# Optimization experiments

Measured on AMD Instinct MI355X. Metric: run time of the kernel, lower is better.

## Reference

```python
import jax, jax.numpy as jnp
import numpy as np

ALPHA = 0.01
BETA = 3e-05
OUT_H, OUT_W = 256, 256
KSIZE, SIGMA = 5, 4.0


def _gaussian_kernel2d(ks=KSIZE, sigma=SIGMA):
    x = jnp.arange(ks, dtype=jnp.float32) - (ks - 1) / 2.0
    g = jnp.exp(-(x * x) / (2.0 * sigma * sigma))
    g = g / g.sum()
    return jnp.outer(g, g)  # [ks, ks]


def _gaussian_blur(maps):
    # maps: [B, H, W]; reflect padding + depthwise 5x5 gaussian (kornia-style GaussianBlur2d)
    k = _gaussian_kernel2d()[None, None]  # [1,1,5,5]
    p = KSIZE // 2
    x = jnp.pad(maps[:, None], ((0, 0), (0, 0), (p, p), (p, p)), mode='reflect')
    y = jax.lax.conv_general_dilated(x, k, (1, 1), 'VALID')
    return y[:, 0]


def _resize_bilinear_align_corners(x, oh, ow):
    # x: [B, h, w] -> [B, oh, ow], torch F.interpolate(mode='bilinear', align_corners=True)
    B, h, w = x.shape
    ys = jnp.linspace(0.0, h - 1.0, oh)
    xs = jnp.linspace(0.0, w - 1.0, ow)
    y0 = jnp.floor(ys).astype(jnp.int32)
    x0 = jnp.floor(xs).astype(jnp.int32)
    y1 = jnp.minimum(y0 + 1, h - 1)
    x1 = jnp.minimum(x0 + 1, w - 1)
    fy = (ys - y0.astype(ys.dtype))[:, None]  # [oh,1]
    fx = (xs - x0.astype(xs.dtype))[None, :]  # [1,ow]
    a = x[:, y0][:, :, x0]
    b = x[:, y0][:, :, x1]
    c = x[:, y1][:, :, x0]
    d = x[:, y1][:, :, x1]
    top = a * (1.0 - fx) + b * fx
    bot = c * (1.0 - fx) + d * fx
    return top * (1.0 - fy) + bot * fy


def setup_inputs() -> dict:
    key = jax.random.key(0)
    k0, k1, k2 = jax.random.split(key, 3)
    B = 256
    return {
        'out0': jax.random.normal(k0, (B, 64, 64), jnp.float32),
        'out1': jax.random.normal(k1, (B, 32, 32), jnp.float32),
        'out2': jax.random.normal(k2, (B, 16, 16), jnp.float32),
    }


def reference(out0, out1, out2):
    outputs = [out0, out1, out2]
    B = out0.shape[0]
    # per-sample max of each scale -> softmax-weighted selection of per-sample weight
    max_vals = jnp.stack([o.reshape(B, -1).max(axis=1) for o in outputs], axis=1)  # [B,3]
    probs = jax.nn.softmax(max_vals, axis=1)
    mask = probs > probs.mean(axis=1, keepdims=True)  # probs > prob_mean
    cnt = mask.sum(axis=1)
    sel_mean = (max_vals * mask).sum(axis=1) / jnp.maximum(cnt, 1)
    total_weights = jnp.where(cnt > 0, jnp.maximum(sel_mean * ALPHA, BETA), BETA)  # [B]
    # multi-scale fusion: bilinear(align_corners=True) upsample to (256,256) and sum
    maps = _resize_bilinear_align_corners(out0, OUT_H, OUT_W)
    maps = maps + _resize_bilinear_align_corners(out1, OUT_H, OUT_W)
    maps = maps + _resize_bilinear_align_corners(out2, OUT_H, OUT_W)
    # gaussian blur then per-sample score. torch takes topk(k=f(total_weights)).values[0],
    # and topk values are sorted descending, so values[0] == max (k / total_weights drop out).
    blurred = _gaussian_blur(maps)
    scores = blurred.reshape(B, -1).max(axis=1)
    del total_weights  # only influenced the (unused) top-k size in the original
    return scores[:, None], maps
```

## Files before the change

### kernel.cpp

```cpp
#include <hip/hip_runtime.h>
#include <math.h>


static constexpr int W  = 256;
static constexpr int QH = 4;

__device__ __forceinline__ int reflect256(int i) {
    if (i < 0) i = -i;
    if (i > 255) i = 510 - i;
    return i;
}

__global__ __launch_bounds__(256, 4) void fused_kernel(
    const float* __restrict__ in0,
    const float* __restrict__ in1,
    const float* __restrict__ in2,
    float* __restrict__ part,
    float* __restrict__ maps)
{
    const int t   = threadIdx.x;
    const int q   = t & 63;
    const int wv  = __builtin_amdgcn_readfirstlane(t >> 6);
    const int bid = blockIdx.x;
    const int b   = bid >> 2;
    const int r0  = (bid & 3) * 64;
    const int rw0 = r0 + wv * 16;
    const int c0  = q * 4;

    __shared__ float s0[64 * 64];
    __shared__ float s1[32 * 32];
    __shared__ float s2[16 * 16];
    __shared__ float red[4];

    {
        const float4* g0 = (const float4*)(in0 + (size_t)b * 4096);
        const float4* g1 = (const float4*)(in1 + (size_t)b * 1024);
        const float4* g2 = (const float4*)(in2 + (size_t)b * 256);
        float4* l0 = (float4*)s0;
        float4* l1 = (float4*)s1;
        float4* l2 = (float4*)s2;
#pragma unroll
        for (int i = 0; i < 4; ++i) l0[t + i * 256] = g0[t + i * 256];
        l1[t] = g1[t];
        if (t < 64) l2[t] = g2[t];
    }
    __syncthreads();

    const float inv255 = 1.0f / 255.0f;
    int x00[4]; float fx0[4];
    int x10[4]; float fx1[4];
    int x20[4]; float fx2[4];
#pragma unroll
    for (int k = 0; k < 4; ++k) {
        const int c = c0 + k;
        int ix = c * 63; x00[k] = ix / 255; fx0[k] = (float)(ix - 255 * x00[k]) * inv255;
        ix = c * 31;     x10[k] = ix / 255; fx1[k] = (float)(ix - 255 * x10[k]) * inv255;
        ix = c * 15;     x20[k] = ix / 255; fx2[k] = (float)(ix - 255 * x20[k]) * inv255;
    }

    auto xq0 = [&](int y, float* o) {
        const float* row = s0 + y * 64;
#pragma unroll
        for (int k = 0; k < 4; ++k) {
            int xa = x00[k], xb = min(xa + 1, 63);
            float a = row[xa], bb = row[xb];
            o[k] = a + fx0[k] * (bb - a);
        }
    };
    auto xq1 = [&](int y, float* o) {
        const float* row = s1 + y * 32;
#pragma unroll
        for (int k = 0; k < 4; ++k) {
            int xa = x10[k], xb = min(xa + 1, 31);
            float a = row[xa], bb = row[xb];
            o[k] = a + fx1[k] * (bb - a);
        }
    };
    auto xq2 = [&](int y, float* o) {
        const float* row = s2 + y * 16;
#pragma unroll
        for (int k = 0; k < 4; ++k) {
            int xa = x20[k], xb = min(xa + 1, 15);
            float a = row[xa], bb = row[xb];
            o[k] = a + fx2[k] * (bb - a);
        }
    };

    auto direct4 = [&](int rn, float* o) {
        const int ry = reflect256(rn);
        int iy0 = ry * 63; int ya0 = iy0 / 255; float fya = (float)(iy0 - 255 * ya0) * inv255; int ya1 = min(ya0 + 1, 63);
        int iy1 = ry * 31; int yb0 = iy1 / 255; float fyb = (float)(iy1 - 255 * yb0) * inv255; int yb1 = min(yb0 + 1, 31);
        int iy2 = ry * 15; int yc0 = iy2 / 255; float fyc = (float)(iy2 - 255 * yc0) * inv255; int yc1 = min(yc0 + 1, 15);
        const float* r0a = s0 + ya0 * 64; const float* r0b = s0 + ya1 * 64;
        const float* r1a = s1 + yb0 * 32; const float* r1b = s1 + yb1 * 32;
        const float* r2a = s2 + yc0 * 16; const float* r2b = s2 + yc1 * 16;
#pragma unroll
        for (int k = 0; k < 4; ++k) {
            int xa = x00[k], xb = min(xa + 1, 63);
            float a = r0a[xa], bv = r0a[xb], cv = r0b[xa], dv = r0b[xb];
            float top = a + fx0[k] * (bv - a);
            float bot = cv + fx0[k] * (dv - cv);
            float v = top + fya * (bot - top);
            xa = x10[k]; xb = min(xa + 1, 31);
            a = r1a[xa]; bv = r1a[xb]; cv = r1b[xa]; dv = r1b[xb];
            top = a + fx1[k] * (bv - a);
            bot = cv + fx1[k] * (dv - cv);
            v += top + fyb * (bot - top);
            xa = x20[k]; xb = min(xa + 1, 15);
            a = r2a[xa]; bv = r2a[xb]; cv = r2b[xa]; dv = r2b[xb];
            top = a + fx2[k] * (bv - a);
            bot = cv + fx2[k] * (dv - cv);
            v += top + fyc * (bot - top);
            o[k] = v;
        }
    };

    const float e1 = expf(-1.0f / 32.0f);
    const float e2 = expf(-4.0f / 32.0f);
    const float nrm = 1.0f + 2.0f * e1 + 2.0f * e2;
    const float gwc = 1.0f / nrm, gwa = e1 / nrm, gwb = e2 / nrm;

    float m0[4], m1[4], m2[4], m3[4], mn[4];
    direct4(rw0 - 2, m0);
    direct4(rw0 - 1, m1);
    direct4(rw0,     m2);
    direct4(rw0 + 1, m3);

    float* __restrict__ mpr = maps + ((size_t)b * W + (size_t)rw0) * W + c0;
    *(float4*)(mpr)     = make_float4(m2[0], m2[1], m2[2], m2[3]);
    *(float4*)(mpr + W) = make_float4(m3[0], m3[1], m3[2], m3[3]);

    int iy, ya, yb, yc, rem0, rem1, rem2;
    float rlo0[4], rhi0[4], rlo1[4], rhi1[4], rlo2[4], rhi2[4];
    iy = (rw0 + 2) * 63; ya = iy / 255; rem0 = iy - 255 * ya; xq0(ya, rlo0); xq0(min(ya + 1, 63), rhi0);
    iy = (rw0 + 2) * 31; yb = iy / 255; rem1 = iy - 255 * yb; xq1(yb, rlo1); xq1(min(yb + 1, 31), rhi1);
    iy = (rw0 + 2) * 15; yc = iy / 255; rem2 = iy - 255 * yc; xq2(yc, rlo2); xq2(min(yc + 1, 15), rhi2);

    float gmax = -INFINITY;

#pragma unroll 4
    for (int i = 0; i < 16; ++i) {
        const int rn = rw0 + 2 + i;
        if (rn <= 255) {
            const float w0 = (float)rem0 * inv255;
            const float w1 = (float)rem1 * inv255;
            const float w2 = (float)rem2 * inv255;
#pragma unroll
            for (int k = 0; k < 4; ++k) {
                float v0 = rlo0[k] + w0 * (rhi0[k] - rlo0[k]);
                float v1 = rlo1[k] + w1 * (rhi1[k] - rlo1[k]);
                float v2 = rlo2[k] + w2 * (rhi2[k] - rlo2[k]);
                mn[k] = v0 + v1 + v2;
            }
            rem0 += 63;
            if (rem0 >= 255) {
                rem0 -= 255; ++ya;
#pragma unroll
                for (int k = 0; k < 4; ++k) rlo0[k] = rhi0[k];
                xq0(min(ya + 1, 63), rhi0);
            }
            rem1 += 31;
            if (rem1 >= 255) {
                rem1 -= 255; ++yb;
#pragma unroll
                for (int k = 0; k < 4; ++k) rlo1[k] = rhi1[k];
                xq1(min(yb + 1, 31), rhi1);
            }
            rem2 += 15;
            if (rem2 >= 255) {
                rem2 -= 255; ++yc;
#pragma unroll
                for (int k = 0; k < 4; ++k) rlo2[k] = rhi2[k];
                xq2(min(yc + 1, 15), rhi2);
            }
        } else {
            direct4(rn, mn);
        }

        if (i < 14)
            *(float4*)(mpr + (size_t)(2 + i) * W) = make_float4(mn[0], mn[1], mn[2], mn[3]);

        float vr0 = gwb * (m0[0] + mn[0]) + gwa * (m1[0] + m3[0]) + gwc * m2[0];
        float vr1 = gwb * (m0[1] + mn[1]) + gwa * (m1[1] + m3[1]) + gwc * m2[1];
        float vr2 = gwb * (m0[2] + mn[2]) + gwa * (m1[2] + m3[2]) + gwc * m2[2];
        float vr3 = gwb * (m0[3] + mn[3]) + gwa * (m1[3] + m3[3]) + gwc * m2[3];
#pragma unroll
        for (int k = 0; k < 4; ++k) { m0[k] = m1[k]; m1[k] = m2[k]; m2[k] = m3[k]; m3[k] = mn[k]; }

        float az = __shfl_up(vr2, 1);
        float aw = __shfl_up(vr3, 1);
        float cx = __shfl_down(vr0, 1);
        float cy = __shfl_down(vr1, 1);
        float a2 = (q == 0)  ? vr2 : az;
        float a3 = (q == 0)  ? vr1 : aw;
        float c4 = (q == 63) ? vr2 : cx;
        float c5 = (q == 63) ? vr1 : cy;
        float o0 = gwc * vr0 + gwa * (a3 + vr1)  + gwb * (a2 + vr2);
        float o1 = gwc * vr1 + gwa * (vr0 + vr2) + gwb * (a3 + vr3);
        float o2 = gwc * vr2 + gwa * (vr1 + vr3) + gwb * (vr0 + c4);
        float o3 = gwc * vr3 + gwa * (vr2 + c4)  + gwb * (vr1 + c5);
        gmax = fmaxf(gmax, fmaxf(fmaxf(o0, o1), fmaxf(o2, o3)));
    }

#pragma unroll
    for (int off = 32; off > 0; off >>= 1)
        gmax = fmaxf(gmax, __shfl_down(gmax, off));
    if (q == 0) red[wv] = gmax;
    __syncthreads();
    if (t == 0)
        part[bid] = fmaxf(fmaxf(red[0], red[1]), fmaxf(red[2], red[3]));
}

__global__ void reduce_kernel(const float* __restrict__ part,
                              float* __restrict__ scores, int B) {
    int i = blockIdx.x * blockDim.x + threadIdx.x;
    if (i < B) {
        float m = part[QH * i];
#pragma unroll
        for (int k = 1; k < QH; ++k) m = fmaxf(m, part[QH * i + k]);
        scores[i] = m;
    }
}

extern "C" void kernel_launch(void* const* d_in, const int* in_sizes, int n_in,
                              void* d_out, int out_size, void* d_ws, size_t ws_size,
                              hipStream_t stream) {
    const float* in0 = (const float*)d_in[0];
    const float* in1 = (const float*)d_in[1];
    const float* in2 = (const float*)d_in[2];
    const int B = in_sizes[0] / (64 * 64);

    float* scores = (float*)d_out;
    float* maps   = (float*)d_out + B;
    float* part   = (float*)d_ws;

    hipLaunchKernelGGL(fused_kernel, dim3(B * QH), dim3(256), 0, stream,
                       in0, in1, in2, part, maps);
    hipLaunchKernelGGL(reduce_kernel, dim3((B + 255) / 256), dim3(256), 0, stream,
                       part, scores, B);
}
```

Measured before the change: 109.4 us.

## Split each sample into eight row bands and stage only needed input rows

Each block now covers 32 output rows instead of 64, with 8 rows per wave, doubling the grid and raising launch bounds to 8 blocks per CU. Only the source rows each band touches are copied into a much smaller LDS buffer, which cuts LDS use and redundant global loads. The halo rows are now produced by the incremental stepping interpolator instead of direct 4-tap evaluation, with a reflect special case for row 0. Per-wave maxima are written straight to the workspace, removing the block barrier, and the reduce kernel now reads 32 partials per sample.

After: 267.4 us. 145% more time.

```diff
diff --git a/kernel.cpp b/kernel.cpp
--- a/kernel.cpp
+++ b/kernel.cpp
@@ -3,7 +3,7 @@
 
 
 static constexpr int W  = 256;
-static constexpr int QH = 4;
+static constexpr int QB = 8;
 
 __device__ __forceinline__ int reflect256(int i) {
     if (i < 0) i = -i;
@@ -11,7 +11,7 @@
     return i;
 }
 
-__global__ __launch_bounds__(256, 4) void fused_kernel(
+__global__ __launch_bounds__(256, 8) void fused_kernel(
     const float* __restrict__ in0,
     const float* __restrict__ in1,
     const float* __restrict__ in2,
@@ -22,27 +22,34 @@
     const int q   = t & 63;
     const int wv  = __builtin_amdgcn_readfirstlane(t >> 6);
     const int bid = blockIdx.x;
-    const int b   = bid >> 2;
-    const int r0  = (bid & 3) * 64;
-    const int rw0 = r0 + wv * 16;
+    const int b   = bid >> 3;
+    const int r0  = (bid & 7) * 32;
+    const int rw0 = r0 + wv * 8;
     const int c0  = q * 4;
 
-    __shared__ float s0[64 * 64];
-    __shared__ float s1[32 * 32];
-    __shared__ float s2[16 * 16];
-    __shared__ float red[4];
+    const int rlo = max(r0 - 2, 0);
+    const int rhi = min(r0 + 33, 255);
+    const int y0lo = (rlo * 63) / 255;
+    const int y1lo = (rlo * 31) / 255;
+    const int y2lo = (rlo * 15) / 255;
+    const int y0hi = min((rhi * 63) / 255 + 1, 63);
+    const int y1hi = min((rhi * 31) / 255 + 1, 31);
+    const int y2hi = min((rhi * 15) / 255 + 1, 15);
+
+    __shared__ float s0[11 * 64];
+    __shared__ float s1[7 * 32];
+    __shared__ float s2[5 * 16];
 
     {
-        const float4* g0 = (const float4*)(in0 + (size_t)b * 4096);
-        const float4* g1 = (const float4*)(in1 + (size_t)b * 1024);
-        const float4* g2 = (const float4*)(in2 + (size_t)b * 256);
-        float4* l0 = (float4*)s0;
-        float4* l1 = (float4*)s1;
-        float4* l2 = (float4*)s2;
-#pragma unroll
-        for (int i = 0; i < 4; ++i) l0[t + i * 256] = g0[t + i * 256];
-        l1[t] = g1[t];
-        if (t < 64) l2[t] = g2[t];
+        const float4* g0 = (const float4*)(in0 + (size_t)b * 4096 + y0lo * 64);
+        const float4* g1 = (const float4*)(in1 + (size_t)b * 1024 + y1lo * 32);
+        const float4* g2 = (const float4*)(in2 + (size_t)b * 256  + y2lo * 16);
+        const int n0 = (y0hi - y0lo + 1) * 16;
+        const int n1 = (y1hi - y1lo + 1) * 8;
+        const int n2 = (y2hi - y2lo + 1) * 4;
+        if (t < n0) ((float4*)s0)[t] = g0[t];
+        if (t < n1) ((float4*)s1)[t] = g1[t];
+        if (t < n2) ((float4*)s2)[t] = g2[t];
     }
     __syncthreads();
 
@@ -59,7 +66,7 @@
     }
 
     auto xq0 = [&](int y, float* o) {
-        const float* row = s0 + y * 64;
+        const float* row = s0 + (y - y0lo) * 64;
 #pragma unroll
         for (int k = 0; k < 4; ++k) {
             int xa = x00[k], xb = min(xa + 1, 63);
@@ -68,7 +75,7 @@
         }
     };
     auto xq1 = [&](int y, float* o) {
-        const float* row = s1 + y * 32;
+        const float* row = s1 + (y - y1lo) * 32;
 #pragma unroll
         for (int k = 0; k < 4; ++k) {
             int xa = x10[k], xb = min(xa + 1, 31);
@@ -77,7 +84,7 @@
         }
     };
     auto xq2 = [&](int y, float* o) {
-        const float* row = s2 + y * 16;
+        const float* row = s2 + (y - y2lo) * 16;
 #pragma unroll
         for (int k = 0; k < 4; ++k) {
             int xa = x20[k], xb = min(xa + 1, 15);
@@ -91,9 +98,9 @@
         int iy0 = ry * 63; int ya0 = iy0 / 255; float fya = (float)(iy0 - 255 * ya0) * inv255; int ya1 = min(ya0 + 1, 63);
         int iy1 = ry * 31; int yb0 = iy1 / 255; float fyb = (float)(iy1 - 255 * yb0) * inv255; int yb1 = min(yb0 + 1, 31);
         int iy2 = ry * 15; int yc0 = iy2 / 255; float fyc = (float)(iy2 - 255 * yc0) * inv255; int yc1 = min(yc0 + 1, 15);
-        const float* r0a = s0 + ya0 * 64; const float* r0b = s0 + ya1 * 64;
-        const float* r1a = s1 + yb0 * 32; const float* r1b = s1 + yb1 * 32;
-        const float* r2a = s2 + yc0 * 16; const float* r2b = s2 + yc1 * 16;
+        const float* r0a = s0 + (ya0 - y0lo) * 64; const float* r0b = s0 + (ya1 - y0lo) * 64;
+        const float* r1a = s1 + (yb0 - y1lo) * 32; const float* r1b = s1 + (yb1 - y1lo) * 32;
+        const float* r2a = s2 + (yc0 - y2lo) * 16; const float* r2b = s2 + (yc1 - y2lo) * 16;
 #pragma unroll
         for (int k = 0; k < 4; ++k) {
             int xa = x00[k], xb = min(xa + 1, 63);
@@ -115,69 +122,81 @@
         }
     };
 
+    int ya, yb, yc, rem0, rem1, rem2;
+    float rl0[4], rh0[4], rl1[4], rh1[4], rl2[4], rh2[4];
+
+    auto init_state = [&](int rn) {
+        int iy;
+        iy = rn * 63; ya = iy / 255; rem0 = iy - 255 * ya; xq0(ya, rl0); xq0(min(ya + 1, 63), rh0);
+        iy = rn * 31; yb = iy / 255; rem1 = iy - 255 * yb; xq1(yb, rl1); xq1(min(yb + 1, 31), rh1);
+        iy = rn * 15; yc = iy / 255; rem2 = iy - 255 * yc; xq2(yc, rl2); xq2(min(yc + 1, 15), rh2);
+    };
+
+    auto step = [&](float* o) {
+        const float w0 = (float)rem0 * inv255;
+        const float w1 = (float)rem1 * inv255;
+        const float w2 = (float)rem2 * inv255;
+#pragma unroll
+        for (int k = 0; k < 4; ++k) {
+            float v0 = rl0[k] + w0 * (rh0[k] - rl0[k]);
+            float v1 = rl1[k] + w1 * (rh1[k] - rl1[k]);
+            float v2 = rl2[k] + w2 * (rh2[k] - rl2[k]);
+            o[k] = v0 + v1 + v2;
+        }
+        rem0 += 63;
+        if (rem0 >= 255) {
+            rem0 -= 255; ++ya;
+#pragma unroll
+            for (int k = 0; k < 4; ++k) rl0[k] = rh0[k];
+            xq0(min(ya + 1, 63), rh0);
+        }
+        rem1 += 31;
+        if (rem1 >= 255) {
+            rem1 -= 255; ++yb;
+#pragma unroll
+            for (int k = 0; k < 4; ++k) rl1[k] = rh1[k];
+            xq1(min(yb + 1, 31), rh1);
+        }
+        rem2 += 15;
+        if (rem2 >= 255) {
+            rem2 -= 255; ++yc;
+#pragma unroll
+            for (int k = 0; k < 4; ++k) rl2[k] = rh2[k];
+            xq2(min(yc + 1, 15), rh2);
+        }
+    };
+
     const float e1 = expf(-1.0f / 32.0f);
     const float e2 = expf(-4.0f / 32.0f);
     const float nrm = 1.0f + 2.0f * e1 + 2.0f * e2;
     const float gwc = 1.0f / nrm, gwa = e1 / nrm, gwb = e2 / nrm;
 
     float m0[4], m1[4], m2[4], m3[4], mn[4];
-    direct4(rw0 - 2, m0);
-    direct4(rw0 - 1, m1);
-    direct4(rw0,     m2);
-    direct4(rw0 + 1, m3);
+    if (rw0 == 0) {
+        direct4(2, m0);
+        direct4(1, m1);
+        direct4(0, m2);
+#pragma unroll
+        for (int k = 0; k < 4; ++k) m3[k] = m1[k];
+        init_state(2);
+    } else {
+        init_state(rw0 - 2);
+        step(m0); step(m1); step(m2); step(m3);
+    }
 
     float* __restrict__ mpr = maps + ((size_t)b * W + (size_t)rw0) * W + c0;
     *(float4*)(mpr)     = make_float4(m2[0], m2[1], m2[2], m2[3]);
     *(float4*)(mpr + W) = make_float4(m3[0], m3[1], m3[2], m3[3]);
 
-    int iy, ya, yb, yc, rem0, rem1, rem2;
-    float rlo0[4], rhi0[4], rlo1[4], rhi1[4], rlo2[4], rhi2[4];
-    iy = (rw0 + 2) * 63; ya = iy / 255; rem0 = iy - 255 * ya; xq0(ya, rlo0); xq0(min(ya + 1, 63), rhi0);
-    iy = (rw0 + 2) * 31; yb = iy / 255; rem1 = iy - 255 * yb; xq1(yb, rlo1); xq1(min(yb + 1, 31), rhi1);
-    iy = (rw0 + 2) * 15; yc = iy / 255; rem2 = iy - 255 * yc; xq2(yc, rlo2); xq2(min(yc + 1, 15), rhi2);
-
     float gmax = -INFINITY;
 
-#pragma unroll 4
-    for (int i = 0; i < 16; ++i) {
+#pragma unroll
+    for (int i = 0; i < 8; ++i) {
         const int rn = rw0 + 2 + i;
-        if (rn <= 255) {
-            const float w0 = (float)rem0 * inv255;
-            const float w1 = (float)rem1 * inv255;
-            const float w2 = (float)rem2 * inv255;
-#pragma unroll
-            for (int k = 0; k < 4; ++k) {
-                float v0 = rlo0[k] + w0 * (rhi0[k] - rlo0[k]);
-                float v1 = rlo1[k] + w1 * (rhi1[k] - rlo1[k]);
-                float v2 = rlo2[k] + w2 * (rhi2[k] - rlo2[k]);
-                mn[k] = v0 + v1 + v2;
-            }
-            rem0 += 63;
-            if (rem0 >= 255) {
-                rem0 -= 255; ++ya;
-#pragma unroll
-                for (int k = 0; k < 4; ++k) rlo0[k] = rhi0[k];
-                xq0(min(ya + 1, 63), rhi0);
-            }
-            rem1 += 31;
-            if (rem1 >= 255) {
-                rem1 -= 255; ++yb;
-#pragma unroll
-                for (int k = 0; k < 4; ++k) rlo1[k] = rhi1[k];
-                xq1(min(yb + 1, 31), rhi1);
-            }
-            rem2 += 15;
-            if (rem2 >= 255) {
-                rem2 -= 255; ++yc;
-#pragma unroll
-                for (int k = 0; k < 4; ++k) rlo2[k] = rhi2[k];
-                xq2(min(yc + 1, 15), rhi2);
-            }
-        } else {
-            direct4(rn, mn);
-        }
-
-        if (i < 14)
+        if (rn <= 255) step(mn);
+        else           direct4(rn, mn);
+
+        if (i < 6)
             *(float4*)(mpr + (size_t)(2 + i) * W) = make_float4(mn[0], mn[1], mn[2], mn[3]);
 
         float vr0 = gwb * (m0[0] + mn[0]) + gwa * (m1[0] + m3[0]) + gwc * m2[0];
@@ -205,19 +224,20 @@
 #pragma unroll
     for (int off = 32; off > 0; off >>= 1)
         gmax = fmaxf(gmax, __shfl_down(gmax, off));
-    if (q == 0) red[wv] = gmax;
-    __syncthreads();
-    if (t == 0)
-        part[bid] = fmaxf(fmaxf(red[0], red[1]), fmaxf(red[2], red[3]));
+    if (q == 0) part[bid * 4 + wv] = gmax;
 }
 
 __global__ void reduce_kernel(const float* __restrict__ part,
                               float* __restrict__ scores, int B) {
     int i = blockIdx.x * blockDim.x + threadIdx.x;
     if (i < B) {
-        float m = part[QH * i];
-#pragma unroll
-        for (int k = 1; k < QH; ++k) m = fmaxf(m, part[QH * i + k]);
+        const float4* p = (const float4*)(part + 32 * i);
+        float m = -INFINITY;
+#pragma unroll
+        for (int k = 0; k < 8; ++k) {
+            float4 v = p[k];
+            m = fmaxf(m, fmaxf(fmaxf(v.x, v.y), fmaxf(v.z, v.w)));
+        }
         scores[i] = m;
     }
 }
@@ -234,7 +254,7 @@
     float* maps   = (float*)d_out + B;
     float* part   = (float*)d_ws;
 
-    hipLaunchKernelGGL(fused_kernel, dim3(B * QH), dim3(256), 0, stream,
+    hipLaunchKernelGGL(fused_kernel, dim3(B * QB), dim3(256), 0, stream,
                        in0, in1, in2, part, maps);
     hipLaunchKernelGGL(reduce_kernel, dim3((B + 255) / 256), dim3(256), 0, stream,
                        part, scores, B);
```
